# Kernel tuning notes

Measured on AMD Instinct MI355X. Metric: run time of the kernel, lower is better.

The kernel has to match this reference:

```python
import jax, jax.numpy as jnp
import numpy as np

LORA_ALPHA = 1
RANK = 16
SCALING = LORA_ALPHA / RANK  # self.lora_alpha / self.r


def setup_inputs() -> dict:
    key = jax.random.key(0)
    ks = jax.random.split(key, 7)
    depth, dim, r = 12, 768, 16
    B, L = 128, 197
    return {
        "x": jax.random.normal(ks[0], (B, L, dim), dtype=jnp.float32),
        "q_lora_A": jax.random.normal(ks[1], (depth, dim, r), dtype=jnp.float32) * 0.02,
        "q_lora_B": jax.random.normal(ks[2], (depth, r, dim), dtype=jnp.float32) * 0.02,
        "k_lora_A": jax.random.normal(ks[3], (depth, dim, r), dtype=jnp.float32) * 0.02,
        "k_lora_B": jax.random.normal(ks[4], (depth, r, dim), dtype=jnp.float32) * 0.02,
        "v_lora_A": jax.random.normal(ks[5], (depth, dim, r), dtype=jnp.float32) * 0.02,
        "v_lora_B": jax.random.normal(ks[6], (depth, r, dim), dtype=jnp.float32) * 0.02,
        "depth_id": 0,
    }


def reference(x, q_lora_A, q_lora_B, k_lora_A, k_lora_B, v_lora_A, v_lora_B, depth_id):
    # Faithful to MomentumLora.forward (not-old / task_id==0 branch):
    # per-depth full-rank deltas q,k,v = A[d] @ B[d]  -> each [dim, dim]
    q = q_lora_A[depth_id] @ q_lora_B[depth_id]
    k = k_lora_A[depth_id] @ k_lora_B[depth_id]
    v = v_lora_A[depth_id] @ v_lora_B[depth_id]
    # concat along last dim -> [dim, 3*dim], scale, then apply to x
    w = jnp.concatenate([q, k, v], axis=-1) * jnp.float32(SCALING)
    lora_value = jnp.einsum("bld,dz->blz", x, w)  # [B, L, 3*dim]
    return lora_value
```

## Files before the change

### kernel.cpp

```cpp
#include <hip/hip_runtime.h>


#define DIM   768
#define RNK   16
#define NCOLS 48
#define XS_STRIDE 52

__global__ __launch_bounds__(192) void lora_stage1(
    const float* __restrict__ x,
    const float* __restrict__ Aq, const float* __restrict__ Ak,
    const float* __restrict__ Av,
    const int* __restrict__ depth_id,
    float* __restrict__ ypart, int kspan, int M)
{
    __shared__ float xs[64 * XS_STRIDE];
    __shared__ float as[48 * NCOLS];

    const int t     = threadIdx.x;
    const int row0  = blockIdx.x * 64;
    const int kbase = blockIdx.y * kspan;

    const int dep = depth_id[0];
    const size_t aoff = (size_t)dep * DIM * RNK;
    const float* Ap0 = Aq + aoff;
    const float* Ap1 = Ak + aoff;
    const float* Ap2 = Av + aoff;

    const int cg = t % 12;
    const int rs = t / 12;

    int xr[4], xk4[4];
    #pragma unroll
    for (int j = 0; j < 4; j++) { int f = t + j * 192; xr[j] = f / 12; xk4[j] = f % 12; }
    int ak_[3], ac4[3];
    const float* abase[3];
    #pragma unroll
    for (int j = 0; j < 3; j++) {
        int f = t + j * 192;
        ak_[j] = f / 12; ac4[j] = f % 12;
        int z = ac4[j] >> 2, cq = ac4[j] & 3;
        const float* Ap = (z == 0) ? Ap0 : ((z == 1) ? Ap1 : Ap2);
        abase[j] = Ap + 4 * cq;
    }

    float acc[4][4];
    #pragma unroll
    for (int i = 0; i < 4; i++)
        #pragma unroll
        for (int c = 0; c < 4; c++) acc[i][c] = 0.f;

    for (int kc = 0; kc < kspan; kc += 48) {
        const int k0 = kbase + kc;
        #pragma unroll
        for (int j = 0; j < 4; j++) {
            const float4 v = *reinterpret_cast<const float4*>(
                &x[(size_t)(row0 + xr[j]) * DIM + k0 + 4 * xk4[j]]);
            *reinterpret_cast<float4*>(&xs[xr[j] * XS_STRIDE + 4 * xk4[j]]) = v;
        }
        #pragma unroll
        for (int j = 0; j < 3; j++) {
            const float4 v = *reinterpret_cast<const float4*>(
                &abase[j][(size_t)(k0 + ak_[j]) * RNK]);
            *reinterpret_cast<float4*>(&as[ak_[j] * NCOLS + 4 * ac4[j]]) = v;
        }
        __syncthreads();
        #pragma unroll 8
        for (int k = 0; k < 48; k++) {
            const float4 av = *reinterpret_cast<const float4*>(&as[k * NCOLS + 4 * cg]);
            #pragma unroll
            for (int i = 0; i < 4; i++) {
                const float xv = xs[(rs + 16 * i) * XS_STRIDE + k];
                acc[i][0] = fmaf(xv, av.x, acc[i][0]);
                acc[i][1] = fmaf(xv, av.y, acc[i][1]);
                acc[i][2] = fmaf(xv, av.z, acc[i][2]);
                acc[i][3] = fmaf(xv, av.w, acc[i][3]);
            }
        }
        __syncthreads();
    }

    const float s = 0.0625f;
    #pragma unroll
    for (int i = 0; i < 4; i++) {
        float4 v;
        v.x = acc[i][0] * s; v.y = acc[i][1] * s;
        v.z = acc[i][2] * s; v.w = acc[i][3] * s;
        *reinterpret_cast<float4*>(
            &ypart[((size_t)blockIdx.y * M + row0 + rs + 16 * i) * NCOLS + 4 * cg]) = v;
    }
}

__global__ __launch_bounds__(256) void lora_stage2(
    const float* __restrict__ yp,
    const float* __restrict__ Bq, const float* __restrict__ Bk,
    const float* __restrict__ Bv,
    const int* __restrict__ depth_id,
    float* __restrict__ out, int nsplit, int M)
{
    __shared__ float Bs[16 * 256];
    __shared__ float Ys[64 * 16];

    const int t    = threadIdx.x;
    const int row0 = blockIdx.x * 64;
    const int col0 = blockIdx.y * 256;
    const int z    = col0 / DIM;
    const int c0z  = col0 - z * DIM;

    const int dep = depth_id[0];
    const float* Bz = ((z == 0) ? Bq : ((z == 1) ? Bk : Bv)) + (size_t)dep * RNK * DIM;

    #pragma unroll
    for (int j = 0; j < 4; j++) {
        int f = t + j * 256;
        int k = f >> 6, c = f & 63;
        *reinterpret_cast<float4*>(&Bs[k * 256 + 4 * c]) =
            *reinterpret_cast<const float4*>(&Bz[(size_t)k * DIM + c0z + 4 * c]);
    }
    {
        int r = t >> 2, q = t & 3;
        size_t base = (size_t)(row0 + r) * NCOLS + z * RNK + 4 * q;
        float4 a = *reinterpret_cast<const float4*>(&yp[base]);
        if (nsplit == 2) {
            const float4 b = *reinterpret_cast<const float4*>(&yp[(size_t)M * NCOLS + base]);
            a.x += b.x; a.y += b.y; a.z += b.z; a.w += b.w;
        }
        *reinterpret_cast<float4*>(&Ys[r * 16 + 4 * q]) = a;
    }
    __syncthreads();

    const int c4 = t & 63;
    const int rs = t >> 6;

    float4 bk[16];
    #pragma unroll
    for (int k = 0; k < 16; k++)
        bk[k] = *reinterpret_cast<const float4*>(&Bs[k * 256 + 4 * c4]);

    #pragma unroll
    for (int i = 0; i < 16; i++) {
        const int r = rs + 4 * i;
        const float* yr = &Ys[r * 16];
        float4 acc; acc.x = acc.y = acc.z = acc.w = 0.f;
        #pragma unroll
        for (int k = 0; k < 16; k++) {
            const float yv = yr[k];
            acc.x = fmaf(yv, bk[k].x, acc.x);
            acc.y = fmaf(yv, bk[k].y, acc.y);
            acc.z = fmaf(yv, bk[k].z, acc.z);
            acc.w = fmaf(yv, bk[k].w, acc.w);
        }
        *reinterpret_cast<float4*>(&out[(size_t)(row0 + r) * (3 * DIM) + col0 + 4 * c4]) = acc;
    }
}

extern "C" void kernel_launch(void* const* d_in, const int* in_sizes, int n_in,
                              void* d_out, int out_size, void* d_ws, size_t ws_size,
                              hipStream_t stream) {
    const float* x  = (const float*)d_in[0];
    const float* Aq = (const float*)d_in[1];
    const float* Bq = (const float*)d_in[2];
    const float* Ak = (const float*)d_in[3];
    const float* Bk = (const float*)d_in[4];
    const float* Av = (const float*)d_in[5];
    const float* Bv = (const float*)d_in[6];
    const int* dep  = (const int*)d_in[7];
    float* out = (float*)d_out;
    float* y   = (float*)d_ws;

    const int M = in_sizes[0] / DIM;
    const size_t y_bytes_one = (size_t)M * NCOLS * sizeof(float);
    const int nsplit = (ws_size >= 2 * y_bytes_one) ? 2 : 1;
    const int kspan = DIM / nsplit;

    lora_stage1<<<dim3(M / 64, nsplit), 192, 0, stream>>>(x, Aq, Ak, Av, dep, y, kspan, M);
    lora_stage2<<<dim3(M / 64, (3 * DIM) / 256), 256, 0, stream>>>(y, Bq, Bk, Bv, dep, out, nsplit, M);
}
```

Before: 338.3 us.

## Enlarge stage1 row tile, vectorize inner loops, add 4-way K split and nontemporal IO

Stage1 now processes 128 rows per block with 8 accumulators per thread and reads x and A tiles as 4-wide vectors from shared memory, which raises register reuse. The K dimension may be split four ways when the workspace allows, restoring parallelism lost to the larger tile. Loads of x and stores of the output use nontemporal hints to avoid cache pollution. Stage2 is rewritten with vector Ys reads and a different row mapping. The risks are higher register pressure and more partial-sum traffic when four splits are used.

```diff
diff --git a/kernel.cpp b/kernel.cpp
--- a/kernel.cpp
+++ b/kernel.cpp
@@ -6,6 +6,8 @@
 #define NCOLS 48
 #define XS_STRIDE 52
 
+typedef float f32x4 __attribute__((ext_vector_type(4)));
+
 __global__ __launch_bounds__(192) void lora_stage1(
     const float* __restrict__ x,
     const float* __restrict__ Aq, const float* __restrict__ Ak,
@@ -13,67 +15,59 @@
     const int* __restrict__ depth_id,
     float* __restrict__ ypart, int kspan, int M)
 {
-    __shared__ float xs[64 * XS_STRIDE];
+    __shared__ float xs[128 * XS_STRIDE];
     __shared__ float as[48 * NCOLS];
 
-    const int t     = threadIdx.x;
-    const int row0  = blockIdx.x * 64;
+    const int t  = threadIdx.x;
+    const int rg = t / 12;
+    const int cg = t % 12;
+    const int row0  = blockIdx.x * 128;
     const int kbase = blockIdx.y * kspan;
 
     const int dep = depth_id[0];
     const size_t aoff = (size_t)dep * DIM * RNK;
-    const float* Ap0 = Aq + aoff;
-    const float* Ap1 = Ak + aoff;
-    const float* Ap2 = Av + aoff;
+    const float* Ab0 = Aq + aoff;
+    const float* Ab1 = Ak + aoff;
+    const float* Ab2 = Av + aoff;
 
-    const int cg = t % 12;
-    const int rs = t / 12;
-
-    int xr[4], xk4[4];
-    #pragma unroll
-    for (int j = 0; j < 4; j++) { int f = t + j * 192; xr[j] = f / 12; xk4[j] = f % 12; }
-    int ak_[3], ac4[3];
-    const float* abase[3];
-    #pragma unroll
-    for (int j = 0; j < 3; j++) {
-        int f = t + j * 192;
-        ak_[j] = f / 12; ac4[j] = f % 12;
-        int z = ac4[j] >> 2, cq = ac4[j] & 3;
-        const float* Ap = (z == 0) ? Ap0 : ((z == 1) ? Ap1 : Ap2);
-        abase[j] = Ap + 4 * cq;
-    }
-
-    float acc[4][4];
-    #pragma unroll
-    for (int i = 0; i < 4; i++)
-        #pragma unroll
-        for (int c = 0; c < 4; c++) acc[i][c] = 0.f;
+    f32x4 acc[8] = {};
 
     for (int kc = 0; kc < kspan; kc += 48) {
         const int k0 = kbase + kc;
         #pragma unroll
-        for (int j = 0; j < 4; j++) {
-            const float4 v = *reinterpret_cast<const float4*>(
-                &x[(size_t)(row0 + xr[j]) * DIM + k0 + 4 * xk4[j]]);
-            *reinterpret_cast<float4*>(&xs[xr[j] * XS_STRIDE + 4 * xk4[j]]) = v;
+        for (int j = 0; j < 8; j++) {
+            const int f = t + j * 192;
+            const int r = f / 12, k4 = f % 12;
+            const f32x4 v = __builtin_nontemporal_load(
+                reinterpret_cast<const f32x4*>(&x[(size_t)(row0 + r) * DIM + k0 + 4 * k4]));
+            *reinterpret_cast<f32x4*>(&xs[r * XS_STRIDE + 4 * k4]) = v;
         }
         #pragma unroll
         for (int j = 0; j < 3; j++) {
-            const float4 v = *reinterpret_cast<const float4*>(
-                &abase[j][(size_t)(k0 + ak_[j]) * RNK]);
-            *reinterpret_cast<float4*>(&as[ak_[j] * NCOLS + 4 * ac4[j]]) = v;
+            const int f = t + j * 192;
+            const int k = f / 12, c4 = f % 12;
+            const int z = c4 >> 2, cq = c4 & 3;
+            const float* Ap = (z == 0) ? Ab0 : ((z == 1) ? Ab1 : Ab2);
+            const f32x4 v = *reinterpret_cast<const f32x4*>(&Ap[(size_t)(k0 + k) * RNK + 4 * cq]);
+            *reinterpret_cast<f32x4*>(&as[k * NCOLS + 4 * c4]) = v;
         }
         __syncthreads();
-        #pragma unroll 8
-        for (int k = 0; k < 48; k++) {
-            const float4 av = *reinterpret_cast<const float4*>(&as[k * NCOLS + 4 * cg]);
+
+        #pragma unroll 2
+        for (int kk = 0; kk < 48; kk += 4) {
+            f32x4 xf[8], af[4];
             #pragma unroll
-            for (int i = 0; i < 4; i++) {
-                const float xv = xs[(rs + 16 * i) * XS_STRIDE + k];
-                acc[i][0] = fmaf(xv, av.x, acc[i][0]);
-                acc[i][1] = fmaf(xv, av.y, acc[i][1]);
-                acc[i][2] = fmaf(xv, av.z, acc[i][2]);
-                acc[i][3] = fmaf(xv, av.w, acc[i][3]);
+            for (int i = 0; i < 8; i++)
+                xf[i] = *reinterpret_cast<const f32x4*>(&xs[(rg + 16 * i) * XS_STRIDE + kk]);
+            #pragma unroll
+            for (int j = 0; j < 4; j++)
+                af[j] = *reinterpret_cast<const f32x4*>(&as[(kk + j) * NCOLS + 4 * cg]);
+            #pragma unroll
+            for (int i = 0; i < 8; i++) {
+                acc[i] += xf[i][0] * af[0];
+                acc[i] += xf[i][1] * af[1];
+                acc[i] += xf[i][2] * af[2];
+                acc[i] += xf[i][3] * af[3];
             }
         }
         __syncthreads();
@@ -81,12 +75,10 @@
 
     const float s = 0.0625f;
     #pragma unroll
-    for (int i = 0; i < 4; i++) {
-        float4 v;
-        v.x = acc[i][0] * s; v.y = acc[i][1] * s;
-        v.z = acc[i][2] * s; v.w = acc[i][3] * s;
-        *reinterpret_cast<float4*>(
-            &ypart[((size_t)blockIdx.y * M + row0 + rs + 16 * i) * NCOLS + 4 * cg]) = v;
+    for (int i = 0; i < 8; i++) {
+        f32x4 v = acc[i] * s;
+        *reinterpret_cast<f32x4*>(
+            &ypart[((size_t)blockIdx.y * M + row0 + rg + 16 * i) * NCOLS + 4 * cg]) = v;
     }
 }
 
@@ -111,45 +103,43 @@
 
     #pragma unroll
     for (int j = 0; j < 4; j++) {
-        int f = t + j * 256;
-        int k = f >> 6, c = f & 63;
-        *reinterpret_cast<float4*>(&Bs[k * 256 + 4 * c]) =
-            *reinterpret_cast<const float4*>(&Bz[(size_t)k * DIM + c0z + 4 * c]);
+        const int f = t + j * 256;
+        const int k = f >> 6, c = f & 63;
+        *reinterpret_cast<f32x4*>(&Bs[k * 256 + 4 * c]) =
+            *reinterpret_cast<const f32x4*>(&Bz[(size_t)k * DIM + c0z + 4 * c]);
     }
     {
-        int r = t >> 2, q = t & 3;
-        size_t base = (size_t)(row0 + r) * NCOLS + z * RNK + 4 * q;
-        float4 a = *reinterpret_cast<const float4*>(&yp[base]);
-        if (nsplit == 2) {
-            const float4 b = *reinterpret_cast<const float4*>(&yp[(size_t)M * NCOLS + base]);
-            a.x += b.x; a.y += b.y; a.z += b.z; a.w += b.w;
-        }
-        *reinterpret_cast<float4*>(&Ys[r * 16 + 4 * q]) = a;
+        const int r = t >> 2, q = t & 3;
+        const size_t base = (size_t)(row0 + r) * NCOLS + z * RNK + 4 * q;
+        f32x4 a = *reinterpret_cast<const f32x4*>(&yp[base]);
+        for (int sp = 1; sp < nsplit; sp++)
+            a += *reinterpret_cast<const f32x4*>(&yp[(size_t)sp * M * NCOLS + base]);
+        *reinterpret_cast<f32x4*>(&Ys[r * 16 + 4 * q]) = a;
     }
     __syncthreads();
 
+    const int w  = t >> 6;
     const int c4 = t & 63;
-    const int rs = t >> 6;
 
-    float4 bk[16];
+    f32x4 bk[16];
     #pragma unroll
     for (int k = 0; k < 16; k++)
-        bk[k] = *reinterpret_cast<const float4*>(&Bs[k * 256 + 4 * c4]);
+        bk[k] = *reinterpret_cast<const f32x4*>(&Bs[k * 256 + 4 * c4]);
 
-    #pragma unroll
+    #pragma unroll 2
     for (int i = 0; i < 16; i++) {
-        const int r = rs + 4 * i;
-        const float* yr = &Ys[r * 16];
-        float4 acc; acc.x = acc.y = acc.z = acc.w = 0.f;
-        #pragma unroll
-        for (int k = 0; k < 16; k++) {
-            const float yv = yr[k];
-            acc.x = fmaf(yv, bk[k].x, acc.x);
-            acc.y = fmaf(yv, bk[k].y, acc.y);
-            acc.z = fmaf(yv, bk[k].z, acc.z);
-            acc.w = fmaf(yv, bk[k].w, acc.w);
-        }
-        *reinterpret_cast<float4*>(&out[(size_t)(row0 + r) * (3 * DIM) + col0 + 4 * c4]) = acc;
+        const int r = 16 * w + i;
+        const f32x4 y0 = *reinterpret_cast<const f32x4*>(&Ys[r * 16 + 0]);
+        const f32x4 y1 = *reinterpret_cast<const f32x4*>(&Ys[r * 16 + 4]);
+        const f32x4 y2 = *reinterpret_cast<const f32x4*>(&Ys[r * 16 + 8]);
+        const f32x4 y3 = *reinterpret_cast<const f32x4*>(&Ys[r * 16 + 12]);
+        f32x4 acc = y0[0] * bk[0];
+        acc += y0[1] * bk[1];  acc += y0[2] * bk[2];  acc += y0[3] * bk[3];
+        acc += y1[0] * bk[4];  acc += y1[1] * bk[5];  acc += y1[2] * bk[6];  acc += y1[3] * bk[7];
+        acc += y2[0] * bk[8];  acc += y2[1] * bk[9];  acc += y2[2] * bk[10]; acc += y2[3] * bk[11];
+        acc += y3[0] * bk[12]; acc += y3[1] * bk[13]; acc += y3[2] * bk[14]; acc += y3[3] * bk[15];
+        __builtin_nontemporal_store(acc,
+            reinterpret_cast<f32x4*>(&out[(size_t)(row0 + r) * (3 * DIM) + col0 + 4 * c4]));
     }
 }
 
@@ -168,10 +158,12 @@
     float* y   = (float*)d_ws;
 
     const int M = in_sizes[0] / DIM;
-    const size_t y_bytes_one = (size_t)M * NCOLS * sizeof(float);
-    const int nsplit = (ws_size >= 2 * y_bytes_one) ? 2 : 1;
+    const size_t y_one = (size_t)M * NCOLS * sizeof(float);
+    int nsplit = 1;
+    if (ws_size >= 4 * y_one) nsplit = 4;
+    else if (ws_size >= 2 * y_one) nsplit = 2;
     const int kspan = DIM / nsplit;
 
-    lora_stage1<<<dim3(M / 64, nsplit), 192, 0, stream>>>(x, Aq, Ak, Av, dep, y, kspan, M);
+    lora_stage1<<<dim3(M / 128, nsplit), 192, 0, stream>>>(x, Aq, Ak, Av, dep, y, kspan, M);
     lora_stage2<<<dim3(M / 64, (3 * DIM) / 256), 256, 0, stream>>>(y, Bq, Bk, Bv, dep, out, nsplit, M);
 }
```

After: 333.8 us. About the same (-1.3%).
